# Kernel optimization log

Measured on AMD Instinct MI355X. Metric: run time of the kernel, lower is better.

Reference implementation:

```python
import jax, jax.numpy as jnp
import numpy as np

B, L, D, E, H, TOP_K = 4, 2048, 1024, 8, 512, 2

def setup_inputs() -> dict:
    key = jax.random.key(0)
    k = jax.random.split(key, 6)
    x = jax.random.normal(k[0], (B, L, D), dtype=jnp.float32)
    gate_w = jax.random.normal(k[1], (D, E), dtype=jnp.float32) * 0.02
    gate_b = jnp.zeros((E,), jnp.float32)
    w1 = jax.random.normal(k[2], (E, D, H), dtype=jnp.float32) * 0.02
    b1 = jnp.zeros((E, H), jnp.float32)
    w2 = jax.random.normal(k[3], (E, H, D), dtype=jnp.float32) * 0.02
    b2 = jnp.zeros((E, D), jnp.float32)
    return {"x": x, "gate_w": gate_w, "gate_b": gate_b,
            "w1": w1, "b1": b1, "w2": w2, "b2": b2}

def reference(x, gate_w, gate_b, w1, b1, w2, b2):
    b, l, d = x.shape
    e = gate_w.shape[1]
    xf = x.reshape(-1, d)                      # [T, D], T = B*L
    t = xf.shape[0]
    # gating (eval mode: clean logits, no noise)
    logits = xf @ gate_w + gate_b              # [T, E]
    top_vals, top_idx = jax.lax.top_k(logits, TOP_K)
    top_gates = jax.nn.softmax(top_vals, axis=-1)
    gates = jnp.zeros((t, e), x.dtype).at[jnp.arange(t)[:, None], top_idx].set(top_gates)
    # per-expert 2-layer MLP computed densely, combined with sparse gates
    h = jax.nn.gelu(jnp.einsum('td,edh->eth', xf, w1) + b1[:, None, :], approximate=False)
    eo = jnp.einsum('eth,ehd->etd', h, w2) + b2[:, None, :]   # [E, T, D]
    out = jnp.einsum('te,etd->td', gates, eo)                 # weighted combine
    return out.reshape(b, l, d)
```

## Files before the change

kernel.cpp:

```cpp
#include <hip/hip_runtime.h>
#include <hip/hip_bf16.h>
#include <stdint.h>

#define B_    4
#define L_    2048
#define T_    8192
#define D_    1024
#define E_    8
#define H_    512

typedef __bf16  bf16x8 __attribute__((ext_vector_type(8)));
typedef float   f32x4  __attribute__((ext_vector_type(4)));
typedef unsigned short ushort_t;

__device__ __forceinline__ ushort_t f2bf(float f) {
    union { float f; unsigned u; } v; v.f = f;
    unsigned u = v.u;
    unsigned r = (u + 0x7fffu + ((u >> 16) & 1u)) >> 16;
    return (ushort_t)r;
}

__device__ __forceinline__ float gelu_exact(float v) {
    return 0.5f * v * (1.0f + erff(v * 0.70710678118654752f));
}

__device__ __forceinline__ void gld_lds16(const void* g, void* l) {
    __attribute__((address_space(3))) uint32_t* lp =
        reinterpret_cast<__attribute__((address_space(3))) uint32_t*>(
            reinterpret_cast<uintptr_t>(l));
    const __attribute__((address_space(1))) uint32_t* gp =
        reinterpret_cast<const __attribute__((address_space(1))) uint32_t*>(
            reinterpret_cast<uintptr_t>(g));
    __builtin_amdgcn_global_load_lds(gp, lp, 16, 0, 0);
}

__global__ __launch_bounds__(256) void transpose_cvt(
    const float* __restrict__ in, ushort_t* __restrict__ out, int R, int C)
{
    __shared__ float tile[32][33];
    const size_t matoff = (size_t)blockIdx.z * R * C;
    const float* src = in + matoff;
    ushort_t* dst = out + matoff;
    const int r0 = blockIdx.y * 32, c0 = blockIdx.x * 32;
    const int tid = threadIdx.x;
    const int lr = tid >> 3;
    const int lc = (tid & 7) * 4;
    float4 v = *(const float4*)(src + (size_t)(r0 + lr) * C + c0 + lc);
    tile[lr][lc+0] = v.x; tile[lr][lc+1] = v.y;
    tile[lr][lc+2] = v.z; tile[lr][lc+3] = v.w;
    __syncthreads();
    ushort4 o;
    o.x = f2bf(tile[lc+0][lr]);
    o.y = f2bf(tile[lc+1][lr]);
    o.z = f2bf(tile[lc+2][lr]);
    o.w = f2bf(tile[lc+3][lr]);
    *(ushort4*)(dst + (size_t)(c0 + lr) * R + r0 + lc) = o;
}

__global__ __launch_bounds__(256) void gating_kernel(
    const float* __restrict__ x, const float* __restrict__ gw,
    const float* __restrict__ gb,
    int* __restrict__ eidx, float* __restrict__ gsel, ushort_t* __restrict__ xbf)
{
    const int wave = threadIdx.x >> 6;
    const int lane = threadIdx.x & 63;
    const int t = blockIdx.x * 4 + wave;
    const float* xr = x + (size_t)t * D_;
    ushort_t* xbr = xbf + (size_t)t * D_;

    float acc[E_];
    #pragma unroll
    for (int e = 0; e < E_; ++e) acc[e] = 0.f;

    #pragma unroll
    for (int j = 0; j < 4; ++j) {
        const int d = j * 256 + lane * 4;
        float4 xv = *(const float4*)(xr + d);
        ushort4 o;
        o.x = f2bf(xv.x); o.y = f2bf(xv.y); o.z = f2bf(xv.z); o.w = f2bf(xv.w);
        *(ushort4*)(xbr + d) = o;
        const float* gr = gw + (size_t)d * E_;
        float xs[4] = {xv.x, xv.y, xv.z, xv.w};
        #pragma unroll
        for (int c = 0; c < 4; ++c) {
            float4 g0 = *(const float4*)(gr + c * 8);
            float4 g1 = *(const float4*)(gr + c * 8 + 4);
            acc[0] += xs[c] * g0.x; acc[1] += xs[c] * g0.y;
            acc[2] += xs[c] * g0.z; acc[3] += xs[c] * g0.w;
            acc[4] += xs[c] * g1.x; acc[5] += xs[c] * g1.y;
            acc[6] += xs[c] * g1.z; acc[7] += xs[c] * g1.w;
        }
    }
    #pragma unroll
    for (int s = 1; s < 64; s <<= 1) {
        #pragma unroll
        for (int e = 0; e < E_; ++e)
            acc[e] += __shfl_xor(acc[e], s, 64);
    }
    if (lane == 0) {
        float v[E_];
        #pragma unroll
        for (int e = 0; e < E_; ++e) v[e] = acc[e] + gb[e];
        int i0 = 0;
        #pragma unroll
        for (int e = 1; e < E_; ++e) if (v[e] > v[i0]) i0 = e;
        int i1 = (i0 == 0) ? 1 : 0;
        #pragma unroll
        for (int e = 0; e < E_; ++e) if (e != i0 && v[e] > v[i1]) i1 = e;
        float g0 = 1.f / (1.f + expf(v[i1] - v[i0]));
        eidx[t] = i0 | (i1 << 8);
        gsel[t] = g0;
    }
}

__global__ __launch_bounds__(256) void bucket_kernel(
    const int* __restrict__ eidx, const float* __restrict__ gsel,
    int* __restrict__ counts, int* __restrict__ btok, float* __restrict__ bgate,
    uint32_t* __restrict__ tpos)
{
    __shared__ int lcnt[E_];
    __shared__ int lbase[E_];
    const int tid = threadIdx.x;
    if (tid < E_) lcnt[tid] = 0;
    __syncthreads();
    const int t = blockIdx.x * 256 + tid;
    const int pk = eidx[t];
    const float g0 = gsel[t];
    const int i0 = pk & 0xff, i1 = (pk >> 8) & 0xff;
    const int p0 = atomicAdd(&lcnt[i0], 1);
    const int p1 = atomicAdd(&lcnt[i1], 1);
    __syncthreads();
    if (tid < E_) lbase[tid] = atomicAdd(&counts[tid], lcnt[tid]);
    __syncthreads();
    const int q0 = lbase[i0] + p0, q1 = lbase[i1] + p1;
    btok[i0 * T_ + q0] = t; bgate[i0 * T_ + q0] = g0;
    btok[i1 * T_ + q1] = t; bgate[i1 * T_ + q1] = 1.f - g0;
    tpos[t] = (uint32_t)((i0 << 13) | q0) | ((uint32_t)((i1 << 13) | q1) << 16);
}

__global__ void prefix_kernel(const int* __restrict__ counts, int* __restrict__ offsets)
{
    if (threadIdx.x == 0 && blockIdx.x == 0) {
        int s = 0;
        for (int e = 0; e < E_; ++e) { offsets[e] = s; s += counts[e]; }
    }
}

__global__ __launch_bounds__(256) void mlp1_kernel(
    const ushort_t* __restrict__ xbf, const ushort_t* __restrict__ w1t,
    const float* __restrict__ b1,
    const int* __restrict__ counts, const int* __restrict__ offsets,
    const int* __restrict__ btok, ushort_t* __restrict__ hbuf)
{
    const int e   = blockIdx.z;
    const int n_e = counts[e];
    const int m0  = blockIdx.x * 64;
    if (m0 >= n_e) return;
    const int n0  = blockIdx.y * 128;
    const int off = offsets[e];

    __shared__ ushort_t As[64 * 64];
    __shared__ ushort_t Bs[128 * 64];

    const int tid  = threadIdx.x;
    const int lane = tid & 63;
    const int wave = tid >> 6;

    const int srow = tid >> 3;
    const int cg   = (tid & 7) ^ (srow & 7);

    const ushort_t* aptr[2];
    #pragma unroll
    for (int i = 0; i < 2; ++i) {
        int m = m0 + i * 32 + srow;
        int tok = btok[e * T_ + (m < n_e ? m : n_e - 1)];
        aptr[i] = xbf + (size_t)tok * D_ + cg * 8;
    }
    const ushort_t* w1e = w1t + (size_t)e * (H_ * D_);
    const ushort_t* bptr[4];
    #pragma unroll
    for (int i = 0; i < 4; ++i)
        bptr[i] = w1e + (size_t)(n0 + i * 32 + srow) * D_ + cg * 8;

    char* aldst = (char*)As + (wave << 10);
    char* bldst = (char*)Bs + (wave << 10);

    const int fm   = lane & 15;
    const int quad = lane >> 4;
    const int wm   = (wave & 1) * 32;
    const int wn   = (wave >> 1) * 64;

    f32x4 acc[2][4];
    #pragma unroll
    for (int i = 0; i < 2; ++i)
        #pragma unroll
        for (int j = 0; j < 4; ++j)
            { acc[i][j][0]=0.f; acc[i][j][1]=0.f; acc[i][j][2]=0.f; acc[i][j][3]=0.f; }

    for (int k0 = 0; k0 < D_; k0 += 64) {
        #pragma unroll
        for (int i = 0; i < 2; ++i)
            gld_lds16(aptr[i] + k0, aldst + (i << 12));
        #pragma unroll
        for (int i = 0; i < 4; ++i)
            gld_lds16(bptr[i] + k0, bldst + (i << 12));
        __syncthreads();
        #pragma unroll
        for (int kk = 0; kk < 2; ++kk) {
            const int grp = kk * 4 + quad;
            bf16x8 af[2], bfr[4];
            #pragma unroll
            for (int i = 0; i < 2; ++i) {
                int ra = wm + i * 16 + fm;
                af[i]  = *(const bf16x8*)((const char*)As + ra * 128 + ((grp ^ (ra & 7)) << 4));
            }
            #pragma unroll
            for (int j = 0; j < 4; ++j) {
                int rb = wn + j * 16 + fm;
                bfr[j] = *(const bf16x8*)((const char*)Bs + rb * 128 + ((grp ^ (rb & 7)) << 4));
            }
            #pragma unroll
            for (int i = 0; i < 2; ++i)
                #pragma unroll
                for (int j = 0; j < 4; ++j)
                    acc[i][j] = __builtin_amdgcn_mfma_f32_16x16x32_bf16(af[i], bfr[j], acc[i][j], 0, 0, 0);
        }
        __syncthreads();
    }

    float bcol[4];
    #pragma unroll
    for (int j = 0; j < 4; ++j)
        bcol[j] = b1[e * H_ + n0 + wn + j * 16 + fm];
    #pragma unroll
    for (int i = 0; i < 2; ++i) {
        #pragma unroll
        for (int r = 0; r < 4; ++r) {
            int m = m0 + wm + i * 16 + quad * 4 + r;
            if (m >= n_e) continue;
            ushort_t* hrow = hbuf + (size_t)(off + m) * H_ + n0;
            #pragma unroll
            for (int j = 0; j < 4; ++j)
                hrow[wn + j * 16 + fm] = f2bf(gelu_exact(acc[i][j][r] + bcol[j]));
        }
    }
}

__global__ __launch_bounds__(256) void mlp2_kernel(
    const ushort_t* __restrict__ hbuf, const ushort_t* __restrict__ w2t,
    const float* __restrict__ b2,
    const int* __restrict__ counts, const int* __restrict__ offsets,
    const float* __restrict__ bgate, ushort_t* __restrict__ obuf)
{
    const int e   = blockIdx.z;
    const int n_e = counts[e];
    const int m0  = blockIdx.x * 64;
    if (m0 >= n_e) return;
    const int n0  = blockIdx.y * 128;
    const int off = offsets[e];

    __shared__ ushort_t As[64 * 64];
    __shared__ ushort_t Bs[128 * 64];

    const int tid  = threadIdx.x;
    const int lane = tid & 63;
    const int wave = tid >> 6;

    const int srow = tid >> 3;
    const int cg   = (tid & 7) ^ (srow & 7);

    const ushort_t* aptr[2];
    #pragma unroll
    for (int i = 0; i < 2; ++i)
        aptr[i] = hbuf + (size_t)(off + m0 + i * 32 + srow) * H_ + cg * 8;
    const ushort_t* w2e = w2t + (size_t)e * (D_ * H_);
    const ushort_t* bptr[4];
    #pragma unroll
    for (int i = 0; i < 4; ++i)
        bptr[i] = w2e + (size_t)(n0 + i * 32 + srow) * H_ + cg * 8;

    char* aldst = (char*)As + (wave << 10);
    char* bldst = (char*)Bs + (wave << 10);

    const int fm   = lane & 15;
    const int quad = lane >> 4;
    const int wm   = (wave & 1) * 32;
    const int wn   = (wave >> 1) * 64;

    f32x4 acc[2][4];
    #pragma unroll
    for (int i = 0; i < 2; ++i)
        #pragma unroll
        for (int j = 0; j < 4; ++j)
            { acc[i][j][0]=0.f; acc[i][j][1]=0.f; acc[i][j][2]=0.f; acc[i][j][3]=0.f; }

    for (int k0 = 0; k0 < H_; k0 += 64) {
        #pragma unroll
        for (int i = 0; i < 2; ++i)
            gld_lds16(aptr[i] + k0, aldst + (i << 12));
        #pragma unroll
        for (int i = 0; i < 4; ++i)
            gld_lds16(bptr[i] + k0, bldst + (i << 12));
        __syncthreads();
        #pragma unroll
        for (int kk = 0; kk < 2; ++kk) {
            const int grp = kk * 4 + quad;
            bf16x8 af[2], bfr[4];
            #pragma unroll
            for (int i = 0; i < 2; ++i) {
                int ra = wm + i * 16 + fm;
                af[i]  = *(const bf16x8*)((const char*)As + ra * 128 + ((grp ^ (ra & 7)) << 4));
            }
            #pragma unroll
            for (int j = 0; j < 4; ++j) {
                int rb = wn + j * 16 + fm;
                bfr[j] = *(const bf16x8*)((const char*)Bs + rb * 128 + ((grp ^ (rb & 7)) << 4));
            }
            #pragma unroll
            for (int i = 0; i < 2; ++i)
                #pragma unroll
                for (int j = 0; j < 4; ++j)
                    acc[i][j] = __builtin_amdgcn_mfma_f32_16x16x32_bf16(af[i], bfr[j], acc[i][j], 0, 0, 0);
        }
        __syncthreads();
    }

    float bcol[4];
    #pragma unroll
    for (int j = 0; j < 4; ++j)
        bcol[j] = b2[e * D_ + n0 + wn + j * 16 + fm];
    #pragma unroll
    for (int i = 0; i < 2; ++i) {
        #pragma unroll
        for (int r = 0; r < 4; ++r) {
            int m = m0 + wm + i * 16 + quad * 4 + r;
            if (m >= n_e) continue;
            float g = bgate[e * T_ + m];
            ushort_t* orow = obuf + (size_t)(off + m) * D_ + n0;
            #pragma unroll
            for (int j = 0; j < 4; ++j)
                orow[wn + j * 16 + fm] = f2bf((acc[i][j][r] + bcol[j]) * g);
        }
    }
}

__global__ __launch_bounds__(256) void combine_kernel(
    const ushort_t* __restrict__ obuf, const uint32_t* __restrict__ tpos,
    const int* __restrict__ offsets, float* __restrict__ out)
{
    const int tid = threadIdx.x;
    const int t = blockIdx.x * 2 + (tid >> 7);
    const int c = (tid & 127) * 8;
    const uint32_t pk = tpos[t];
    const int e0 = (pk >> 13) & 7, p0 = pk & 0x1fff;
    const int e1 = (pk >> 29) & 7, p1 = (pk >> 16) & 0x1fff;
    const size_t s0 = (size_t)(offsets[e0] + p0) * D_ + c;
    const size_t s1 = (size_t)(offsets[e1] + p1) * D_ + c;
    bf16x8 a = *(const bf16x8*)(obuf + s0);
    bf16x8 b = *(const bf16x8*)(obuf + s1);
    float4 o0, o1;
    o0.x = (float)a[0] + (float)b[0];
    o0.y = (float)a[1] + (float)b[1];
    o0.z = (float)a[2] + (float)b[2];
    o0.w = (float)a[3] + (float)b[3];
    o1.x = (float)a[4] + (float)b[4];
    o1.y = (float)a[5] + (float)b[5];
    o1.z = (float)a[6] + (float)b[6];
    o1.w = (float)a[7] + (float)b[7];
    float* orow = out + (size_t)t * D_ + c;
    *(float4*)(orow)     = o0;
    *(float4*)(orow + 4) = o1;
}

extern "C" void kernel_launch(void* const* d_in, const int* in_sizes, int n_in,
                              void* d_out, int out_size, void* d_ws, size_t ws_size,
                              hipStream_t stream)
{
    const float* x  = (const float*)d_in[0];
    const float* gw = (const float*)d_in[1];
    const float* gb = (const float*)d_in[2];
    const float* w1 = (const float*)d_in[3];
    const float* b1 = (const float*)d_in[4];
    const float* w2 = (const float*)d_in[5];
    const float* b2 = (const float*)d_in[6];
    float* out = (float*)d_out;

    char* ws = (char*)d_ws;
    int*   counts  = (int*)ws;
    int*   offsets = counts + 8;
    int*   btok    = (int*)(ws + 256);
    float* bgate   = (float*)(ws + 256 + (size_t)E_*T_*4);
    size_t p = 256 + 2ull * E_ * T_ * 4;
    int*      eidx = (int*)(ws + p);      p += (size_t)T_ * 4;
    float*    gsel = (float*)(ws + p);    p += (size_t)T_ * 4;
    uint32_t* tpos = (uint32_t*)(ws + p); p += (size_t)T_ * 4;
    ushort_t* xbf  = (ushort_t*)(ws + p); p += (size_t)T_*D_*2;
    ushort_t* w1t  = (ushort_t*)(ws + p); p += (size_t)E_*H_*D_*2;
    ushort_t* w2t  = (ushort_t*)(ws + p); p += (size_t)E_*D_*H_*2;
    ushort_t* hbuf = (ushort_t*)(ws + p); p += ((size_t)2*T_+128)*H_*2;
    ushort_t* obuf = (ushort_t*)(ws + p);

    (void)hipMemsetAsync(counts, 0, 64, stream);

    transpose_cvt<<<dim3(H_/32, D_/32, E_), 256, 0, stream>>>(w1, w1t, D_, H_);
    transpose_cvt<<<dim3(D_/32, H_/32, E_), 256, 0, stream>>>(w2, w2t, H_, D_);
    gating_kernel<<<T_/4, 256, 0, stream>>>(x, gw, gb, eidx, gsel, xbf);
    bucket_kernel<<<T_/256, 256, 0, stream>>>(eidx, gsel, counts, btok, bgate, tpos);
    prefix_kernel<<<1, 64, 0, stream>>>(counts, offsets);
    mlp1_kernel<<<dim3(T_/64, H_/128, E_), 256, 0, stream>>>(
        xbf, w1t, b1, counts, offsets, btok, hbuf);
    mlp2_kernel<<<dim3(T_/64, D_/128, E_), 256, 0, stream>>>(
        hbuf, w2t, b2, counts, offsets, bgate, obuf);
    combine_kernel<<<T_/2, 256, 0, stream>>>(obuf, tpos, offsets, out);
}
```

Before: 238.4 us.

## Double-buffer LDS tiles in expert GEMMs and merge weight transpose launches

Both expert MLP GEMM kernels now use two LDS buffers. Each iteration issues the async global-to-LDS loads for the next K tile before computing on the current one, which drops one barrier per iteration and overlaps memory traffic with MFMA work. The two weight transpose/convert launches are folded into a single launch that picks w1 or w2 from the block index, saving a kernel launch. The cost is doubled LDS per block (about 48KB), which may lower occupancy.

Result: faster. 232.2 us (-2.6%).

```diff
diff --git a/kernel.cpp b/kernel.cpp
--- a/kernel.cpp
+++ b/kernel.cpp
@@ -34,14 +34,24 @@
     __builtin_amdgcn_global_load_lds(gp, lp, 16, 0, 0);
 }
 
-__global__ __launch_bounds__(256) void transpose_cvt(
-    const float* __restrict__ in, ushort_t* __restrict__ out, int R, int C)
+__global__ __launch_bounds__(256) void transpose_cvt2(
+    const float* __restrict__ w1, const float* __restrict__ w2,
+    ushort_t* __restrict__ o1, ushort_t* __restrict__ o2)
 {
     __shared__ float tile[32][33];
-    const size_t matoff = (size_t)blockIdx.z * R * C;
-    const float* src = in + matoff;
-    ushort_t* dst = out + matoff;
-    const int r0 = blockIdx.y * 32, c0 = blockIdx.x * 32;
+    const int mz = blockIdx.y;
+    const float* src; ushort_t* dst; int C, R, sh;
+    if (mz < E_) {
+        src = w1 + (size_t)mz * D_ * H_; dst = o1 + (size_t)mz * D_ * H_;
+        R = D_; C = H_; sh = 4;
+    } else {
+        const int m = mz - E_;
+        src = w2 + (size_t)m * D_ * H_;  dst = o2 + (size_t)m * D_ * H_;
+        R = H_; C = D_; sh = 5;
+    }
+    const int bx = blockIdx.x & ((1 << sh) - 1);
+    const int by = blockIdx.x >> sh;
+    const int r0 = by * 32, c0 = bx * 32;
     const int tid = threadIdx.x;
     const int lr = tid >> 3;
     const int lc = (tid & 7) * 4;
@@ -159,8 +169,8 @@
     const int n0  = blockIdx.y * 128;
     const int off = offsets[e];
 
-    __shared__ ushort_t As[64 * 64];
-    __shared__ ushort_t Bs[128 * 64];
+    __shared__ ushort_t As[2][64 * 64];
+    __shared__ ushort_t Bs[2][128 * 64];
 
     const int tid  = threadIdx.x;
     const int lane = tid & 63;
@@ -182,9 +192,6 @@
     for (int i = 0; i < 4; ++i)
         bptr[i] = w1e + (size_t)(n0 + i * 32 + srow) * D_ + cg * 8;
 
-    char* aldst = (char*)As + (wave << 10);
-    char* bldst = (char*)Bs + (wave << 10);
-
     const int fm   = lane & 15;
     const int quad = lane >> 4;
     const int wm   = (wave & 1) * 32;
@@ -197,14 +204,27 @@
         for (int j = 0; j < 4; ++j)
             { acc[i][j][0]=0.f; acc[i][j][1]=0.f; acc[i][j][2]=0.f; acc[i][j][3]=0.f; }
 
+    #define STAGE1(bufi, koff)                                              \
+        do {                                                                \
+            char* al_ = (char*)(&As[bufi][0]) + (wave << 10);               \
+            char* bl_ = (char*)(&Bs[bufi][0]) + (wave << 10);               \
+            _Pragma("unroll")                                               \
+            for (int i_ = 0; i_ < 2; ++i_)                                  \
+                gld_lds16(aptr[i_] + (koff), al_ + (i_ << 12));             \
+            _Pragma("unroll")                                               \
+            for (int i_ = 0; i_ < 4; ++i_)                                  \
+                gld_lds16(bptr[i_] + (koff), bl_ + (i_ << 12));             \
+        } while (0)
+
+    STAGE1(0, 0);
+    __syncthreads();
+
+    int buf = 0;
     for (int k0 = 0; k0 < D_; k0 += 64) {
-        #pragma unroll
-        for (int i = 0; i < 2; ++i)
-            gld_lds16(aptr[i] + k0, aldst + (i << 12));
-        #pragma unroll
-        for (int i = 0; i < 4; ++i)
-            gld_lds16(bptr[i] + k0, bldst + (i << 12));
-        __syncthreads();
+        const bool more = (k0 + 64 < D_);
+        if (more) STAGE1(buf ^ 1, k0 + 64);
+        const char* Ab = (const char*)(&As[buf][0]);
+        const char* Bb = (const char*)(&Bs[buf][0]);
         #pragma unroll
         for (int kk = 0; kk < 2; ++kk) {
             const int grp = kk * 4 + quad;
@@ -212,12 +232,12 @@
             #pragma unroll
             for (int i = 0; i < 2; ++i) {
                 int ra = wm + i * 16 + fm;
-                af[i]  = *(const bf16x8*)((const char*)As + ra * 128 + ((grp ^ (ra & 7)) << 4));
+                af[i]  = *(const bf16x8*)(Ab + ra * 128 + ((grp ^ (ra & 7)) << 4));
             }
             #pragma unroll
             for (int j = 0; j < 4; ++j) {
                 int rb = wn + j * 16 + fm;
-                bfr[j] = *(const bf16x8*)((const char*)Bs + rb * 128 + ((grp ^ (rb & 7)) << 4));
+                bfr[j] = *(const bf16x8*)(Bb + rb * 128 + ((grp ^ (rb & 7)) << 4));
             }
             #pragma unroll
             for (int i = 0; i < 2; ++i)
@@ -225,8 +245,10 @@
                 for (int j = 0; j < 4; ++j)
                     acc[i][j] = __builtin_amdgcn_mfma_f32_16x16x32_bf16(af[i], bfr[j], acc[i][j], 0, 0, 0);
         }
-        __syncthreads();
-    }
+        if (more) __syncthreads();
+        buf ^= 1;
+    }
+    #undef STAGE1
 
     float bcol[4];
     #pragma unroll
@@ -259,8 +281,8 @@
     const int n0  = blockIdx.y * 128;
     const int off = offsets[e];
 
-    __shared__ ushort_t As[64 * 64];
-    __shared__ ushort_t Bs[128 * 64];
+    __shared__ ushort_t As[2][64 * 64];
+    __shared__ ushort_t Bs[2][128 * 64];
 
     const int tid  = threadIdx.x;
     const int lane = tid & 63;
@@ -279,9 +301,6 @@
     for (int i = 0; i < 4; ++i)
         bptr[i] = w2e + (size_t)(n0 + i * 32 + srow) * H_ + cg * 8;
 
-    char* aldst = (char*)As + (wave << 10);
-    char* bldst = (char*)Bs + (wave << 10);
-
     const int fm   = lane & 15;
     const int quad = lane >> 4;
     const int wm   = (wave & 1) * 32;
@@ -294,14 +313,27 @@
         for (int j = 0; j < 4; ++j)
             { acc[i][j][0]=0.f; acc[i][j][1]=0.f; acc[i][j][2]=0.f; acc[i][j][3]=0.f; }
 
+    #define STAGE2(bufi, koff)                                              \
+        do {                                                                \
+            char* al_ = (char*)(&As[bufi][0]) + (wave << 10);               \
+            char* bl_ = (char*)(&Bs[bufi][0]) + (wave << 10);               \
+            _Pragma("unroll")                                               \
+            for (int i_ = 0; i_ < 2; ++i_)                                  \
+                gld_lds16(aptr[i_] + (koff), al_ + (i_ << 12));             \
+            _Pragma("unroll")                                               \
+            for (int i_ = 0; i_ < 4; ++i_)                                  \
+                gld_lds16(bptr[i_] + (koff), bl_ + (i_ << 12));             \
+        } while (0)
+
+    STAGE2(0, 0);
+    __syncthreads();
+
+    int buf = 0;
     for (int k0 = 0; k0 < H_; k0 += 64) {
-        #pragma unroll
-        for (int i = 0; i < 2; ++i)
-            gld_lds16(aptr[i] + k0, aldst + (i << 12));
-        #pragma unroll
-        for (int i = 0; i < 4; ++i)
-            gld_lds16(bptr[i] + k0, bldst + (i << 12));
-        __syncthreads();
+        const bool more = (k0 + 64 < H_);
+        if (more) STAGE2(buf ^ 1, k0 + 64);
+        const char* Ab = (const char*)(&As[buf][0]);
+        const char* Bb = (const char*)(&Bs[buf][0]);
         #pragma unroll
         for (int kk = 0; kk < 2; ++kk) {
             const int grp = kk * 4 + quad;
@@ -309,12 +341,12 @@
             #pragma unroll
             for (int i = 0; i < 2; ++i) {
                 int ra = wm + i * 16 + fm;
-                af[i]  = *(const bf16x8*)((const char*)As + ra * 128 + ((grp ^ (ra & 7)) << 4));
+                af[i]  = *(const bf16x8*)(Ab + ra * 128 + ((grp ^ (ra & 7)) << 4));
             }
             #pragma unroll
             for (int j = 0; j < 4; ++j) {
                 int rb = wn + j * 16 + fm;
-                bfr[j] = *(const bf16x8*)((const char*)Bs + rb * 128 + ((grp ^ (rb & 7)) << 4));
+                bfr[j] = *(const bf16x8*)(Bb + rb * 128 + ((grp ^ (rb & 7)) << 4));
             }
             #pragma unroll
             for (int i = 0; i < 2; ++i)
@@ -322,8 +354,10 @@
                 for (int j = 0; j < 4; ++j)
                     acc[i][j] = __builtin_amdgcn_mfma_f32_16x16x32_bf16(af[i], bfr[j], acc[i][j], 0, 0, 0);
         }
-        __syncthreads();
-    }
+        if (more) __syncthreads();
+        buf ^= 1;
+    }
+    #undef STAGE2
 
     float bcol[4];
     #pragma unroll
@@ -402,8 +436,7 @@
 
     (void)hipMemsetAsync(counts, 0, 64, stream);
 
-    transpose_cvt<<<dim3(H_/32, D_/32, E_), 256, 0, stream>>>(w1, w1t, D_, H_);
-    transpose_cvt<<<dim3(D_/32, H_/32, E_), 256, 0, stream>>>(w2, w2t, H_, D_);
+    transpose_cvt2<<<dim3(512, 16), 256, 0, stream>>>(w1, w2, w1t, w2t);
     gating_kernel<<<T_/4, 256, 0, stream>>>(x, gw, gb, eidx, gsel, xbf);
     bucket_kernel<<<T_/256, 256, 0, stream>>>(eidx, gsel, counts, btok, bgate, tpos);
     prefix_kernel<<<1, 64, 0, stream>>>(counts, offsets);
```
